# Optimization experiments

Hardware: AMD Instinct MI355X
Metric: run time of the kernel (lower is better)

## Reference

```python
import jax, jax.numpy as jnp
import numpy as np

B, SS, T, D, H = 512, 4, 64, 300, 256  # batch, sentences/sample, words/sentence, wordvec, hidden


def setup_inputs() -> dict:
    key = jax.random.key(0)
    ks = jax.random.split(key, 17)
    s = 0.05
    rn = lambda k, shape: (jax.random.normal(k, shape, jnp.float32) * s)
    return dict(
        x=jax.random.normal(ks[0], (B, SS, T, D), jnp.float32),
        # gru1: GRU(300 -> 256), PyTorch gate order (r, z, n)
        w_ih1=rn(ks[1], (3 * H, D)), w_hh1=rn(ks[2], (3 * H, H)),
        b_ih1=rn(ks[3], (3 * H,)), b_hh1=rn(ks[4], (3 * H,)),
        # gru2: bidirectional GRU(256 -> 256), forward + backward directions
        w_ih2f=rn(ks[5], (3 * H, H)), w_hh2f=rn(ks[6], (3 * H, H)),
        b_ih2f=rn(ks[7], (3 * H,)), b_hh2f=rn(ks[8], (3 * H,)),
        w_ih2b=rn(ks[9], (3 * H, H)), w_hh2b=rn(ks[10], (3 * H, H)),
        b_ih2b=rn(ks[11], (3 * H,)), b_hh2b=rn(ks[12], (3 * H,)),
        # classifier: Linear(512,256) -> LeakyReLU(0.1) -> Linear(256,2)
        wc1=rn(ks[13], (H, 2 * H)), bc1=rn(ks[14], (H,)),
        wc2=rn(ks[15], (2, H)), bc2=rn(ks[16], (2,)),
    )


def _gru_final_hidden(x, w_ih, w_hh, b_ih, b_hh):
    # x: [N, T, D] -> final hidden state [N, H]; PyTorch GRU math, gate order r,z,n
    xg = jnp.einsum('ntd,gd->tng', x, w_ih) + b_ih  # [T, N, 3H], input gates precomputed
    h0 = jnp.zeros((x.shape[0], w_hh.shape[1]), x.dtype)

    def step(h, xg_t):
        hg = h @ w_hh.T + b_hh
        xr, xz, xn = jnp.split(xg_t, 3, axis=-1)
        hr, hz, hn = jnp.split(hg, 3, axis=-1)
        r = jax.nn.sigmoid(xr + hr)
        z = jax.nn.sigmoid(xz + hz)
        n = jnp.tanh(xn + r * hn)
        return (1.0 - z) * n + z * h, None

    hT, _ = jax.lax.scan(step, h0, xg)
    return hT


def _gru_cell_zero_h(x, w_ih, b_ih, b_hh):
    # gru2 is called with seq_len=1 and h0=0, so each direction is one cell step
    # (W_hh @ 0 == 0, only the hidden biases survive)
    xg = x @ w_ih.T + b_ih
    xr, xz, xn = jnp.split(xg, 3, axis=-1)
    br, bz, bn = jnp.split(b_hh, 3)
    r = jax.nn.sigmoid(xr + br)
    z = jax.nn.sigmoid(xz + bz)
    n = jnp.tanh(xn + r * bn)
    return (1.0 - z) * n


def reference(x, w_ih1, w_hh1, b_ih1, b_hh1,
              w_ih2f, w_hh2f, b_ih2f, b_hh2f,
              w_ih2b, w_hh2b, b_ih2b, b_hh2b,
              wc1, bc1, wc2, bc2):
    Bn, S, Tn, Dn = x.shape
    # integrate_words: gru1 over each sentence's words, keep final hidden
    h1 = _gru_final_hidden(x.reshape(Bn * S, Tn, Dn), w_ih1, w_hh1, b_ih1, b_hh1)
    h1 = h1.reshape(Bn, S, -1)  # [B, SS, H]
    # integrate_sentences: bidir gru2 with batch=SS, seq_len=1; out[SS//2] is kept,
    # and with seq_len=1 that output depends only on the middle sentence's embedding
    mid = h1[:, S // 2, :]  # [B, H]
    hf = _gru_cell_zero_h(mid, w_ih2f, b_ih2f, b_hh2f)
    hb = _gru_cell_zero_h(mid, w_ih2b, b_ih2b, b_hh2b)
    emb = jnp.concatenate([hf, hb], axis=-1)  # [B, 2H]
    pre = emb @ wc1.T + bc1
    hidden = jnp.where(pre >= 0, pre, 0.1 * pre)  # LeakyReLU(0.1)
    logits = hidden @ wc2.T + bc2  # [B, 2]
    return logits
```

## Files before the change

### kernel.cpp

```cpp
#include <hip/hip_runtime.h>
#include <hip/hip_bf16.h>

typedef unsigned short u16;
typedef unsigned int u32;
using short8 = __attribute__((ext_vector_type(8))) short;
using f32x4  = __attribute__((ext_vector_type(4))) float;

#define T_   64
#define D_   300
#define H_   256
#define G_   768
#define NROW 512
#define M_   (NROW * T_)
#define KP_  320

__device__ __forceinline__ float bf2f(u16 v) {
    union { u32 u; float f; } x; x.u = ((u32)v) << 16; return x.f;
}
__device__ __forceinline__ float bf2f_lo(u32 w) {
    union { u32 u; float f; } x; x.u = w << 16; return x.f;
}
__device__ __forceinline__ float bf2f_hi(u32 w) {
    union { u32 u; float f; } x; x.u = w & 0xFFFF0000u; return x.f;
}
__device__ __forceinline__ u16 f2bf(float f) {
    union { u32 u; float f; } x; x.f = f;
    u32 u = x.u;
    u32 r = (u + 0x7FFFu + ((u >> 16) & 1u)) >> 16;
    return (u16)r;
}
__device__ __forceinline__ float frcp(float x) {
    float r; asm("v_rcp_f32 %0, %1" : "=v"(r) : "v"(x)); return r;
}
__device__ __forceinline__ float fsigm(float x) { return frcp(1.f + __expf(-x)); }
__device__ __forceinline__ float ftanh(float x) {
    return 1.f - 2.f * frcp(1.f + __expf(2.f * x));
}
__device__ __forceinline__ float sigm(float x) { return 1.f / (1.f + expf(-x)); }

__global__ __launch_bounds__(256) void kx_cast(
    const float* __restrict__ x, u16* __restrict__ xb)
{
    const int gid = blockIdx.x * 256 + threadIdx.x;
    const int row = gid / 40, seg = gid - row * 40;
    const int k0 = seg * 8;
    const int n = row >> 6, t = row & 63;
    const float* src = x + (size_t)(n * 256 + 128 + t) * D_;
    union { u16 h[8]; uint4 q; } u;
    if (k0 + 8 <= D_) {
        const float4 a = *reinterpret_cast<const float4*>(src + k0);
        const float4 b = *reinterpret_cast<const float4*>(src + k0 + 4);
        u.h[0] = f2bf(a.x); u.h[1] = f2bf(a.y); u.h[2] = f2bf(a.z); u.h[3] = f2bf(a.w);
        u.h[4] = f2bf(b.x); u.h[5] = f2bf(b.y); u.h[6] = f2bf(b.z); u.h[7] = f2bf(b.w);
    } else {
#pragma unroll
        for (int e = 0; e < 8; ++e)
            u.h[e] = (k0 + e < D_) ? f2bf(src[k0 + e]) : (u16)0;
    }
    *reinterpret_cast<uint4*>(&xb[(size_t)row * KP_ + k0]) = u.q;
}

__global__ __launch_bounds__(256) void k0_prep(
    const float* __restrict__ w_ih1, const float* __restrict__ w_hh1,
    const float* __restrict__ b_ih1, const float* __restrict__ b_hh1,
    const float* __restrict__ w2f, const float* __restrict__ w2b,
    const float* __restrict__ wc1,
    u16* __restrict__ wihb, u16* __restrict__ whpk,
    u16* __restrict__ w2ft, u16* __restrict__ w2bt, u16* __restrict__ wc1t,
    float* __restrict__ biasc)
{
    int y = blockIdx.y;
    int tid = blockIdx.x * 256 + threadIdx.x;
    if (y == 0) {
        if (tid < G_ * KP_) {
            int g = tid / KP_, k = tid % KP_;
            wihb[tid] = (k < D_) ? f2bf(w_ih1[g * D_ + k]) : (u16)0;
        }
    } else if (y == 1) {
        if (tid < 48 * 8 * 64) {
            int lane = tid & 63;
            int ks = (tid >> 6) & 7;
            int nt = tid >> 9;
            int g  = nt * 16 + (lane & 15);
            int kb = ks * 32 + ((lane >> 4) << 3);
            union { u16 h[8]; uint4 q; } u;
#pragma unroll
            for (int e = 0; e < 8; ++e) u.h[e] = f2bf(w_hh1[g * H_ + kb + e]);
            *reinterpret_cast<uint4*>(&whpk[(size_t)tid * 8]) = u.q;
        }
    } else if (y == 2 || y == 3) {
        if (tid < G_ * H_) {
            int k = tid / G_, g = tid % G_;
            const float* src = (y == 2) ? w2f : w2b;
            u16* dst = (y == 2) ? w2ft : w2bt;
            dst[tid] = f2bf(src[g * H_ + k]);
        }
    } else {
        if (tid < 512 * 256) {
            int k = tid / 256, o = tid % 256;
            wc1t[tid] = f2bf(wc1[o * 512 + k]);
        }
        if (tid < G_)
            biasc[tid] = b_ih1[tid] + (tid < 2 * H_ ? b_hh1[tid] : 0.f);
    }
}

__global__ __launch_bounds__(256) void k1_xgemm(
    const u16* __restrict__ xb, const u16* __restrict__ wihb,
    const float* __restrict__ biasc, u16* __restrict__ xgp)
{
    __shared__ alignas(16) u16 As[128 * 40];
    __shared__ alignas(16) u16 Bs[128 * 40];
    const int tid = threadIdx.x;
    const int l = tid & 63, wv = tid >> 6;
    const int wrow = wv >> 1, wcol = wv & 1;
    const int row0 = blockIdx.x * 128, col0 = blockIdx.y * 128;

    f32x4 acc[4][4];
#pragma unroll
    for (int i = 0; i < 4; ++i)
#pragma unroll
        for (int j = 0; j < 4; ++j) acc[i][j] = (f32x4){0.f, 0.f, 0.f, 0.f};

    const int ar = tid >> 1, ah = tid & 1;
    const u16* xrow  = xb + (size_t)(row0 + ar) * KP_;
    const u16* wrowp = wihb + (size_t)(col0 + ar) * KP_;

    for (int k0 = 0; k0 < KP_; k0 += 32) {
        *reinterpret_cast<uint4*>(&As[ar * 40 + ah * 16]) =
            *reinterpret_cast<const uint4*>(xrow + k0 + ah * 16);
        *reinterpret_cast<uint4*>(&As[ar * 40 + ah * 16 + 8]) =
            *reinterpret_cast<const uint4*>(xrow + k0 + ah * 16 + 8);
        *reinterpret_cast<uint4*>(&Bs[ar * 40 + ah * 16]) =
            *reinterpret_cast<const uint4*>(wrowp + k0 + ah * 16);
        *reinterpret_cast<uint4*>(&Bs[ar * 40 + ah * 16 + 8]) =
            *reinterpret_cast<const uint4*>(wrowp + k0 + ah * 16 + 8);
        __syncthreads();

        short8 af[4], bf[4];
#pragma unroll
        for (int fi = 0; fi < 4; ++fi)
            af[fi] = *reinterpret_cast<const short8*>(
                &As[(wrow * 64 + fi * 16 + (l & 15)) * 40 + ((l >> 4) << 3)]);
#pragma unroll
        for (int fj = 0; fj < 4; ++fj)
            bf[fj] = *reinterpret_cast<const short8*>(
                &Bs[(wcol * 64 + fj * 16 + (l & 15)) * 40 + ((l >> 4) << 3)]);
#pragma unroll
        for (int fi = 0; fi < 4; ++fi)
#pragma unroll
            for (int fj = 0; fj < 4; ++fj)
                acc[fi][fj] = __builtin_amdgcn_mfma_f32_16x16x32_bf16(
                    af[fi], bf[fj], acc[fi][fj], 0, 0, 0);
        __syncthreads();
    }

    float bias[4];
#pragma unroll
    for (int fj = 0; fj < 4; ++fj)
        bias[fj] = biasc[col0 + wcol * 64 + fj * 16 + (l & 15)];
#pragma unroll
    for (int fi = 0; fi < 4; ++fi)
#pragma unroll
        for (int fj = 0; fj < 4; ++fj) {
            const int cg = col0 + wcol * 64 + fj * 16 + (l & 15);
            const int gate = cg >> 8, unit = cg & 255;
            const int wv8 = unit >> 5, a = (unit >> 4) & 1, c = unit & 15;
#pragma unroll
            for (int q = 0; q < 4; ++q) {
                const int row = row0 + wrow * 64 + fi * 16 + ((l >> 4) << 2) + q;
                const int t = row & 63, n = row >> 6;
                const size_t idx =
                    (((size_t)t * NROW + n) * 128 + wv8 * 16 + c) * 6 + a * 3 + gate;
                xgp[idx] = f2bf(acc[fi][fj][q] + bias[fj]);
            }
        }
}

__global__ __launch_bounds__(512)
__attribute__((amdgpu_waves_per_eu(2, 2)))
void k2_gru(const u16* __restrict__ xgp, const u16* __restrict__ whpk,
            const float* __restrict__ b_hh, float* __restrict__ mid)
{
    extern __shared__ u16 smem[];
    u16* wl = smem;
    u16* hb = smem + 48 * 2 * 64 * 8;
    const int tid = threadIdx.x;
    const int l = tid & 63, wv = tid >> 6;
    const int n0 = blockIdx.x * 16;
    const int col = l & 15, rgrp = l >> 4;
    const int arow = col, klo = rgrp << 3;

    short8 wr[6][6];
#pragma unroll
    for (int gt = 0; gt < 3; ++gt)
#pragma unroll
        for (int a = 0; a < 2; ++a) {
            const int nt = gt * 16 + wv * 2 + a;
#pragma unroll
            for (int ks = 0; ks < 6; ++ks)
                wr[gt * 2 + a][ks] = *reinterpret_cast<const short8*>(
                    &whpk[(size_t)((nt * 8 + ks) * 64 + l) * 8]);
        }
    asm volatile("" :
        "+a"(wr[0][0]),"+a"(wr[0][1]),"+a"(wr[0][2]),"+a"(wr[0][3]),"+a"(wr[0][4]),"+a"(wr[0][5]),
        "+a"(wr[1][0]),"+a"(wr[1][1]),"+a"(wr[1][2]),"+a"(wr[1][3]),"+a"(wr[1][4]),"+a"(wr[1][5]),
        "+a"(wr[2][0]),"+a"(wr[2][1]),"+a"(wr[2][2]),"+a"(wr[2][3]),"+a"(wr[2][4]),"+a"(wr[2][5]));
    asm volatile("" :
        "+a"(wr[3][0]),"+a"(wr[3][1]),"+a"(wr[3][2]),"+a"(wr[3][3]),"+a"(wr[3][4]),"+a"(wr[3][5]),
        "+a"(wr[4][0]),"+a"(wr[4][1]),"+a"(wr[4][2]),"+a"(wr[4][3]),"+a"(wr[4][4]),"+a"(wr[4][5]),
        "+a"(wr[5][0]),"+a"(wr[5][1]),"+a"(wr[5][2]),"+a"(wr[5][3]),"+a"(wr[5][4]),"+a"(wr[5][5]));

    for (int c = tid; c < 48 * 2 * 64; c += 512) {
        const int nt = c >> 7, j = (c >> 6) & 1, ll = c & 63;
        *reinterpret_cast<uint4*>(&wl[(size_t)c * 8]) =
            *reinterpret_cast<const uint4*>(
                &whpk[(size_t)((nt * 8 + 6 + j) * 64 + ll) * 8]);
    }
    for (int i = tid; i < 2 * 16 * 264 / 2; i += 512) ((u32*)hb)[i] = 0;

    float bhn[2];
    u32 xo[4];
#pragma unroll
    for (int a = 0; a < 2; ++a)
        bhn[a] = b_hh[512 + wv * 32 + a * 16 + col];
#pragma unroll
    for (int q = 0; q < 4; ++q)
        xo[q] = ((u32)(n0 + rgrp * 4 + q) * 128 + wv * 16 + col) * 6;
    float h[2][4] = {};

    __syncthreads();

    int p = 0;
    for (int t = 0; t < T_; ++t) {
        u32 pw0[4], pw1[4], pw2[4];
        const u16* xt = xgp + (size_t)t * ((size_t)NROW * 128 * 6);
#pragma unroll
        for (int q = 0; q < 4; ++q) {
            const u32* pp = reinterpret_cast<const u32*>(xt + xo[q]);
            pw0[q] = pp[0]; pw1[q] = pp[1]; pw2[q] = pp[2];
        }

        const u16* hbr = hb + p * (16 * 264);
        f32x4 acc[6];
#pragma unroll
        for (int m = 0; m < 6; ++m) acc[m] = (f32x4){0.f, 0.f, 0.f, 0.f};
        __builtin_amdgcn_s_setprio(1);
#pragma unroll
        for (int ks = 0; ks < 6; ++ks) {
            const short8 afr = *reinterpret_cast<const short8*>(
                &hbr[arow * 264 + ks * 32 + klo]);
#pragma unroll
            for (int m = 0; m < 6; ++m)
                acc[m] = __builtin_amdgcn_mfma_f32_16x16x32_bf16(
                    afr, wr[m][ks], acc[m], 0, 0, 0);
        }
#pragma unroll
        for (int ks = 6; ks < 8; ++ks) {
            const short8 afr = *reinterpret_cast<const short8*>(
                &hbr[arow * 264 + ks * 32 + klo]);
#pragma unroll
            for (int gt = 0; gt < 3; ++gt)
#pragma unroll
                for (int a = 0; a < 2; ++a) {
                    const int nt2 = (gt * 16 + wv * 2 + a) * 2 + (ks - 6);
                    const short8 bfr = *reinterpret_cast<const short8*>(
                        &wl[(size_t)(nt2 * 64 + l) * 8]);
                    acc[gt * 2 + a] = __builtin_amdgcn_mfma_f32_16x16x32_bf16(
                        afr, bfr, acc[gt * 2 + a], 0, 0, 0);
                }
        }
        __builtin_amdgcn_s_setprio(0);

        u16* hbw = hb + (p ^ 1) * (16 * 264);
#pragma unroll
        for (int q = 0; q < 4; ++q) {
            {
                const float rg = fsigm(bf2f_lo(pw0[q]) + acc[0][q]);
                const float zg = fsigm(bf2f_hi(pw0[q]) + acc[2][q]);
                const float ng = ftanh(bf2f_lo(pw1[q]) + rg * (acc[4][q] + bhn[0]));
                h[0][q] = zg * (h[0][q] - ng) + ng;
                hbw[(rgrp * 4 + q) * 264 + wv * 32 + col] = f2bf(h[0][q]);
            }
            {
                const float rg = fsigm(bf2f_hi(pw1[q]) + acc[1][q]);
                const float zg = fsigm(bf2f_lo(pw2[q]) + acc[3][q]);
                const float ng = ftanh(bf2f_hi(pw2[q]) + rg * (acc[5][q] + bhn[1]));
                h[1][q] = zg * (h[1][q] - ng) + ng;
                hbw[(rgrp * 4 + q) * 264 + wv * 32 + 16 + col] = f2bf(h[1][q]);
            }
        }

        asm volatile("s_waitcnt lgkmcnt(0)" ::: "memory");
        __builtin_amdgcn_sched_barrier(0);
        __builtin_amdgcn_s_barrier();
        __builtin_amdgcn_sched_barrier(0);
        p ^= 1;
    }

#pragma unroll
    for (int a = 0; a < 2; ++a)
#pragma unroll
        for (int q = 0; q < 4; ++q)
            mid[(size_t)(n0 + rgrp * 4 + q) * H_ + wv * 32 + a * 16 + col] = h[a][q];
}

__global__ __launch_bounds__(256) void k3_head(
    const float* __restrict__ mid,
    const u16* __restrict__ w2ft, const u16* __restrict__ w2bt,
    const float* __restrict__ b_ih2f, const float* __restrict__ b_hh2f,
    const float* __restrict__ b_ih2b, const float* __restrict__ b_hh2b,
    const u16* __restrict__ wc1t, const float* __restrict__ bc1,
    const float* __restrict__ wc2, const float* __restrict__ bc2,
    float* __restrict__ out)
{
    __shared__ float m[4][H_];
    __shared__ float xg2[2][4][G_];
    __shared__ float emb[4][512];
    __shared__ float hid[4][H_];
    int tid = threadIdx.x;
    int r0 = blockIdx.x * 4;

    for (int i = tid; i < 4 * H_; i += 256) {
        int r = i >> 8, k = i & 255;
        m[r][k] = mid[(size_t)(r0 + r) * H_ + k];
    }
    __syncthreads();

    const int g0 = tid, g1 = tid + 256, g2 = tid + 512;
    float bf0 = b_ih2f[g0] + b_hh2f[g0];
    float bf1 = b_ih2f[g1] + b_hh2f[g1];
    float bf2v = b_ih2f[g2];
    float bb0 = b_ih2b[g0] + b_hh2b[g0];
    float bb1 = b_ih2b[g1] + b_hh2b[g1];
    float bb2v = b_ih2b[g2];
    float af[4][3], ab[4][3];
#pragma unroll
    for (int r = 0; r < 4; ++r) {
        af[r][0] = bf0; af[r][1] = bf1; af[r][2] = bf2v;
        ab[r][0] = bb0; ab[r][1] = bb1; ab[r][2] = bb2v;
    }
#pragma unroll 4
    for (int k = 0; k < H_; ++k) {
        float wf0 = bf2f(w2ft[k * G_ + g0]);
        float wf1 = bf2f(w2ft[k * G_ + g1]);
        float wf2 = bf2f(w2ft[k * G_ + g2]);
        float wb0 = bf2f(w2bt[k * G_ + g0]);
        float wb1 = bf2f(w2bt[k * G_ + g1]);
        float wb2 = bf2f(w2bt[k * G_ + g2]);
#pragma unroll
        for (int r = 0; r < 4; ++r) {
            float mm = m[r][k];
            af[r][0] += mm * wf0; af[r][1] += mm * wf1; af[r][2] += mm * wf2;
            ab[r][0] += mm * wb0; ab[r][1] += mm * wb1; ab[r][2] += mm * wb2;
        }
    }
#pragma unroll
    for (int r = 0; r < 4; ++r) {
        xg2[0][r][g0] = af[r][0]; xg2[0][r][g1] = af[r][1]; xg2[0][r][g2] = af[r][2];
        xg2[1][r][g0] = ab[r][0]; xg2[1][r][g1] = ab[r][1]; xg2[1][r][g2] = ab[r][2];
    }
    __syncthreads();

    {
        const int j = tid;
        float bnf = b_hh2f[512 + j], bnb = b_hh2b[512 + j];
#pragma unroll
        for (int r = 0; r < 4; ++r) {
            float rg = sigm(xg2[0][r][j]);
            float zg = sigm(xg2[0][r][256 + j]);
            float ng = tanhf(xg2[0][r][512 + j] + rg * bnf);
            emb[r][j] = (1.f - zg) * ng;
            rg = sigm(xg2[1][r][j]);
            zg = sigm(xg2[1][r][256 + j]);
            ng = tanhf(xg2[1][r][512 + j] + rg * bnb);
            emb[r][256 + j] = (1.f - zg) * ng;
        }
    }
    __syncthreads();

    {
        const int o = tid;
        float acc[4];
        float b = bc1[o];
#pragma unroll
        for (int r = 0; r < 4; ++r) acc[r] = b;
#pragma unroll 4
        for (int k = 0; k < 512; ++k) {
            float w = bf2f(wc1t[k * H_ + o]);
#pragma unroll
            for (int r = 0; r < 4; ++r) acc[r] += emb[r][k] * w;
        }
#pragma unroll
        for (int r = 0; r < 4; ++r) {
            float pre = acc[r];
            hid[r][o] = pre >= 0.f ? pre : 0.1f * pre;
        }
    }
    __syncthreads();

    {
        int grp = tid >> 5, lane = tid & 31;
        int r = grp >> 1, cc = grp & 1;
        float s = 0.f;
        for (int k = lane; k < H_; k += 32) s += hid[r][k] * wc2[cc * H_ + k];
#pragma unroll
        for (int msk = 16; msk >= 1; msk >>= 1) s += __shfl_xor(s, msk, 32);
        if (lane == 0) out[(size_t)(r0 + r) * 2 + cc] = s + bc2[cc];
    }
}

extern "C" void kernel_launch(void* const* d_in, const int* in_sizes, int n_in,
                              void* d_out, int out_size, void* d_ws, size_t ws_size,
                              hipStream_t stream)
{
    const float* x      = (const float*)d_in[0];
    const float* w_ih1  = (const float*)d_in[1];
    const float* w_hh1  = (const float*)d_in[2];
    const float* b_ih1  = (const float*)d_in[3];
    const float* b_hh1  = (const float*)d_in[4];
    const float* w_ih2f = (const float*)d_in[5];
    const float* b_ih2f = (const float*)d_in[7];
    const float* b_hh2f = (const float*)d_in[8];
    const float* w_ih2b = (const float*)d_in[9];
    const float* b_ih2b = (const float*)d_in[11];
    const float* b_hh2b = (const float*)d_in[12];
    const float* wc1    = (const float*)d_in[13];
    const float* bc1    = (const float*)d_in[14];
    const float* wc2    = (const float*)d_in[15];
    const float* bc2    = (const float*)d_in[16];
    float* out = (float*)d_out;

    char* p = (char*)d_ws;
    u16* xgp  = (u16*)p;  p += (size_t)M_ * 768 * 2;
    u16* xb   = (u16*)p;  p += (size_t)M_ * KP_ * 2;
    u16* wihb = (u16*)p;  p += (size_t)G_ * KP_ * 2;
    u16* whpk = (u16*)p;  p += (size_t)48 * 8 * 64 * 8 * 2;
    u16* w2ft = (u16*)p;  p += (size_t)G_ * H_ * 2;
    u16* w2bt = (u16*)p;  p += (size_t)G_ * H_ * 2;
    u16* wc1t = (u16*)p;  p += (size_t)512 * 256 * 2;
    float* mid = (float*)p; p += (size_t)NROW * H_ * 4;
    float* biasc = (float*)p; p += (size_t)G_ * 4;

    kx_cast<<<M_ * 40 / 256, 256, 0, stream>>>(x, xb);
    k0_prep<<<dim3(960, 5), 256, 0, stream>>>(w_ih1, w_hh1, b_ih1, b_hh1,
                                              w_ih2f, w_ih2b, wc1,
                                              wihb, whpk, w2ft, w2bt, wc1t, biasc);
    k1_xgemm<<<dim3(M_ / 128, G_ / 128), 256, 0, stream>>>(xb, wihb, biasc, xgp);
    const int k2_lds = (48 * 2 * 64 * 8 + 2 * 16 * 264) * 2;
    k2_gru<<<32, 512, k2_lds, stream>>>(xgp, whpk, b_hh1, mid);
    k3_head<<<128, 256, 0, stream>>>(mid, w2ft, w2bt, b_ih2f, b_hh2f,
                                     b_ih2b, b_hh2b, wc1t, bc1, wc2, bc2, out);
}
```

Baseline: 255.0 us.

## Halve GRU rows per block, shuffle gate outputs, prefetch next-step input gates

The recurrent GRU kernel now handles 8 sequences per block instead of 16, launching 64 blocks rather than 32 so more CUs share the serial recurrence. The MFMA tiles still span 16 rows, so half of each tile is wasted, and lane shuffles redistribute gate accumulators so every lane runs the pointwise gate math for a single unit. The input-gate GEMM output is repacked into 32-bit words that pair adjacent units, and the next timestep's input gates are prefetched into registers one step ahead to hide global load latency. The extra shuffles and the wasted half of each MFMA tile are the cost.

```diff
diff --git a/kernel.cpp b/kernel.cpp
--- a/kernel.cpp
+++ b/kernel.cpp
@@ -107,7 +107,7 @@
 
 __global__ __launch_bounds__(256) void k1_xgemm(
     const u16* __restrict__ xb, const u16* __restrict__ wihb,
-    const float* __restrict__ biasc, u16* __restrict__ xgp)
+    const float* __restrict__ biasc, u32* __restrict__ xgw)
 {
     __shared__ alignas(16) u16 As[128 * 40];
     __shared__ alignas(16) u16 Bs[128 * 40];
@@ -162,24 +162,25 @@
 #pragma unroll
     for (int fi = 0; fi < 4; ++fi)
 #pragma unroll
-        for (int fj = 0; fj < 4; ++fj) {
-            const int cg = col0 + wcol * 64 + fj * 16 + (l & 15);
-            const int gate = cg >> 8, unit = cg & 255;
-            const int wv8 = unit >> 5, a = (unit >> 4) & 1, c = unit & 15;
+        for (int fjp = 0; fjp < 2; ++fjp) {
+            const int cg0 = col0 + wcol * 64 + fjp * 32;
+            const int g = cg0 >> 8;
+            const int wv8 = (cg0 & 255) >> 5;
+            const int word = g * 128 + wv8 * 16 + (l & 15);
 #pragma unroll
             for (int q = 0; q < 4; ++q) {
                 const int row = row0 + wrow * 64 + fi * 16 + ((l >> 4) << 2) + q;
                 const int t = row & 63, n = row >> 6;
-                const size_t idx =
-                    (((size_t)t * NROW + n) * 128 + wv8 * 16 + c) * 6 + a * 3 + gate;
-                xgp[idx] = f2bf(acc[fi][fj][q] + bias[fj]);
+                const u32 lo = f2bf(acc[fi][2 * fjp][q] + bias[2 * fjp]);
+                const u32 hi = f2bf(acc[fi][2 * fjp + 1][q] + bias[2 * fjp + 1]);
+                xgw[((size_t)t * NROW + n) * 384 + word] = lo | (hi << 16);
             }
         }
 }
 
 __global__ __launch_bounds__(512)
 __attribute__((amdgpu_waves_per_eu(2, 2)))
-void k2_gru(const u16* __restrict__ xgp, const u16* __restrict__ whpk,
+void k2_gru(const u32* __restrict__ xgw, const u16* __restrict__ whpk,
             const float* __restrict__ b_hh, float* __restrict__ mid)
 {
     extern __shared__ u16 smem[];
@@ -187,9 +188,12 @@
     u16* hb = smem + 48 * 2 * 64 * 8;
     const int tid = threadIdx.x;
     const int l = tid & 63, wv = tid >> 6;
-    const int n0 = blockIdx.x * 16;
-    const int col = l & 15, rgrp = l >> 4;
-    const int arow = col, klo = rgrp << 3;
+    const int n0 = blockIdx.x * 8;
+    const int c = l & 15, rgrp = l >> 4;
+    const int arow = c, klo = rgrp << 3;
+    const int aSel = rgrp >> 1;
+    const int rbase = (rgrp & 1) * 4;
+    const int u = wv * 32 + aSel * 16 + c;
 
     short8 wr[6][6];
 #pragma unroll
@@ -211,34 +215,40 @@
         "+a"(wr[4][0]),"+a"(wr[4][1]),"+a"(wr[4][2]),"+a"(wr[4][3]),"+a"(wr[4][4]),"+a"(wr[4][5]),
         "+a"(wr[5][0]),"+a"(wr[5][1]),"+a"(wr[5][2]),"+a"(wr[5][3]),"+a"(wr[5][4]),"+a"(wr[5][5]));
 
-    for (int c = tid; c < 48 * 2 * 64; c += 512) {
-        const int nt = c >> 7, j = (c >> 6) & 1, ll = c & 63;
-        *reinterpret_cast<uint4*>(&wl[(size_t)c * 8]) =
+    for (int cc = tid; cc < 48 * 2 * 64; cc += 512) {
+        const int nt = cc >> 7, j = (cc >> 6) & 1, ll = cc & 63;
+        *reinterpret_cast<uint4*>(&wl[(size_t)cc * 8]) =
             *reinterpret_cast<const uint4*>(
                 &whpk[(size_t)((nt * 8 + 6 + j) * 64 + ll) * 8]);
     }
     for (int i = tid; i < 2 * 16 * 264 / 2; i += 512) ((u32*)hb)[i] = 0;
 
-    float bhn[2];
+    const float bhn = b_hh[512 + u];
     u32 xo[4];
 #pragma unroll
-    for (int a = 0; a < 2; ++a)
-        bhn[a] = b_hh[512 + wv * 32 + a * 16 + col];
-#pragma unroll
     for (int q = 0; q < 4; ++q)
-        xo[q] = ((u32)(n0 + rgrp * 4 + q) * 128 + wv * 16 + col) * 6;
-    float h[2][4] = {};
+        xo[q] = (u32)(n0 + rbase + q) * 384 + wv * 16 + c;
+    float h[4] = {0.f, 0.f, 0.f, 0.f};
+    const u32 stepw = (u32)NROW * 384;
+
+    u32 xa[3][4], xn2[3][4];
+#pragma unroll
+    for (int q = 0; q < 4; ++q) {
+        xa[0][q] = xgw[xo[q]];
+        xa[1][q] = xgw[xo[q] + 128];
+        xa[2][q] = xgw[xo[q] + 256];
+    }
 
     __syncthreads();
 
     int p = 0;
     for (int t = 0; t < T_; ++t) {
-        u32 pw0[4], pw1[4], pw2[4];
-        const u16* xt = xgp + (size_t)t * ((size_t)NROW * 128 * 6);
+        const u32 tb = (u32)(t + 1 < T_ ? t + 1 : T_ - 1) * stepw;
 #pragma unroll
         for (int q = 0; q < 4; ++q) {
-            const u32* pp = reinterpret_cast<const u32*>(xt + xo[q]);
-            pw0[q] = pp[0]; pw1[q] = pp[1]; pw2[q] = pp[2];
+            xn2[0][q] = xgw[tb + xo[q]];
+            xn2[1][q] = xgw[tb + xo[q] + 128];
+            xn2[2][q] = xgw[tb + xo[q] + 256];
         }
 
         const u16* hbr = hb + p * (16 * 264);
@@ -272,24 +282,34 @@
         }
         __builtin_amdgcn_s_setprio(0);
 
+        float vr[4], vz[4], vn[4];
+#pragma unroll
+        for (int q = 0; q < 4; ++q) {
+            const float r1 = __shfl(acc[1][q], l & 31);
+            const float z1 = __shfl(acc[3][q], l & 31);
+            const float n1 = __shfl(acc[5][q], l & 31);
+            vr[q] = (l < 32) ? acc[0][q] : r1;
+            vz[q] = (l < 32) ? acc[2][q] : z1;
+            vn[q] = (l < 32) ? acc[4][q] : n1;
+        }
+
         u16* hbw = hb + (p ^ 1) * (16 * 264);
 #pragma unroll
         for (int q = 0; q < 4; ++q) {
-            {
-                const float rg = fsigm(bf2f_lo(pw0[q]) + acc[0][q]);
-                const float zg = fsigm(bf2f_hi(pw0[q]) + acc[2][q]);
-                const float ng = ftanh(bf2f_lo(pw1[q]) + rg * (acc[4][q] + bhn[0]));
-                h[0][q] = zg * (h[0][q] - ng) + ng;
-                hbw[(rgrp * 4 + q) * 264 + wv * 32 + col] = f2bf(h[0][q]);
-            }
-            {
-                const float rg = fsigm(bf2f_hi(pw1[q]) + acc[1][q]);
-                const float zg = fsigm(bf2f_lo(pw2[q]) + acc[3][q]);
-                const float ng = ftanh(bf2f_hi(pw2[q]) + rg * (acc[5][q] + bhn[1]));
-                h[1][q] = zg * (h[1][q] - ng) + ng;
-                hbw[(rgrp * 4 + q) * 264 + wv * 32 + 16 + col] = f2bf(h[1][q]);
-            }
-        }
+            const float xr = aSel ? bf2f_hi(xa[0][q]) : bf2f_lo(xa[0][q]);
+            const float xz = aSel ? bf2f_hi(xa[1][q]) : bf2f_lo(xa[1][q]);
+            const float xn = aSel ? bf2f_hi(xa[2][q]) : bf2f_lo(xa[2][q]);
+            const float rg = fsigm(xr + vr[q]);
+            const float zg = fsigm(xz + vz[q]);
+            const float ng = ftanh(xn + rg * (vn[q] + bhn));
+            h[q] = zg * (h[q] - ng) + ng;
+            hbw[(rbase + q) * 264 + u] = f2bf(h[q]);
+        }
+
+#pragma unroll
+        for (int g = 0; g < 3; ++g)
+#pragma unroll
+            for (int q = 0; q < 4; ++q) xa[g][q] = xn2[g][q];
 
         asm volatile("s_waitcnt lgkmcnt(0)" ::: "memory");
         __builtin_amdgcn_sched_barrier(0);
@@ -299,10 +319,8 @@
     }
 
 #pragma unroll
-    for (int a = 0; a < 2; ++a)
-#pragma unroll
-        for (int q = 0; q < 4; ++q)
-            mid[(size_t)(n0 + rgrp * 4 + q) * H_ + wv * 32 + a * 16 + col] = h[a][q];
+    for (int q = 0; q < 4; ++q)
+        mid[(size_t)(n0 + rbase + q) * H_ + u] = h[q];
 }
 
 __global__ __launch_bounds__(256) void k3_head(
@@ -432,7 +450,7 @@
     float* out = (float*)d_out;
 
     char* p = (char*)d_ws;
-    u16* xgp  = (u16*)p;  p += (size_t)M_ * 768 * 2;
+    u32* xgw  = (u32*)p;  p += (size_t)M_ * 384 * 4;
     u16* xb   = (u16*)p;  p += (size_t)M_ * KP_ * 2;
     u16* wihb = (u16*)p;  p += (size_t)G_ * KP_ * 2;
     u16* whpk = (u16*)p;  p += (size_t)48 * 8 * 64 * 8 * 2;
@@ -446,9 +464,9 @@
     k0_prep<<<dim3(960, 5), 256, 0, stream>>>(w_ih1, w_hh1, b_ih1, b_hh1,
                                               w_ih2f, w_ih2b, wc1,
                                               wihb, whpk, w2ft, w2bt, wc1t, biasc);
-    k1_xgemm<<<dim3(M_ / 128, G_ / 128), 256, 0, stream>>>(xb, wihb, biasc, xgp);
+    k1_xgemm<<<dim3(M_ / 128, G_ / 128), 256, 0, stream>>>(xb, wihb, biasc, xgw);
     const int k2_lds = (48 * 2 * 64 * 8 + 2 * 16 * 264) * 2;
-    k2_gru<<<32, 512, k2_lds, stream>>>(xgp, whpk, b_hh1, mid);
+    k2_gru<<<64, 512, k2_lds, stream>>>(xgw, whpk, b_hh1, mid);
     k3_head<<<128, 256, 0, stream>>>(mid, w2ft, w2bt, b_ih2f, b_hh2f,
                                      b_ih2b, b_hh2b, wc1t, bc1, wc2, bc2, out);
 }
```

Result: faster. 233.7 us (-8.3%).
